# Kernel optimization log

Measured on AMD Instinct MI355X. Metric: run time of the kernel, lower is better.

## Reference

```python
import jax, jax.numpy as jnp
import numpy as np

N_COLS = 4096
N_ROWS = 4096
H = 64          # args.hidden1
S = 2           # per-edge supp feature count (cv_supp/vc_supp dim 0)
S_VO = 2        # vo_supp feature dim
S_CO = 2        # co_supp feature dim
EDGE_DENSITY = 0.03


def setup_inputs() -> dict:
    key = jax.random.key(0)
    ks = jax.random.split(key, 20)
    col_hidden = jax.random.normal(ks[0], (N_COLS, H), jnp.float32)
    row_hidden = jax.random.normal(ks[1], (N_ROWS, H), jnp.float32)
    obj_hidden = jax.random.normal(ks[2], (1, H), jnp.float32)
    # sparse bipartite adjacency encoded in supp[0] != 0 (as in the TF code)
    mask = jax.random.bernoulli(ks[3], EDGE_DENSITY, (N_ROWS, N_COLS))
    cv_supp = jax.random.normal(ks[4], (S, N_ROWS, N_COLS), jnp.float32) * mask[None]
    vc_supp = jnp.transpose(cv_supp, (0, 2, 1))  # [S, ncols, nrows]
    vo_supp = jax.random.normal(ks[5], (N_COLS, S_VO), jnp.float32)
    co_supp = jax.random.normal(ks[6], (N_ROWS, S_CO), jnp.float32)
    w = 0.05
    W_vo = jax.random.normal(ks[7], (2 * H, H), jnp.float32) * w
    W_oc = jax.random.normal(ks[8], (2 * H, H), jnp.float32) * w
    W_vc = jax.random.normal(ks[9], (2 * H, H), jnp.float32) * w
    W_co = jax.random.normal(ks[10], (2 * H, H), jnp.float32) * w
    W_ov = jax.random.normal(ks[11], (2 * H, H), jnp.float32) * w
    W_cv = jax.random.normal(ks[12], (2 * H, H), jnp.float32) * w
    # attention scorer nets: Dense(concat_dim -> 1) + sigmoid
    w_attn_vo = jax.random.normal(ks[13], (2 * H + S_VO, 1), jnp.float32) * 0.1
    b_attn_vo = jnp.zeros((), jnp.float32)
    w_attn_co = jax.random.normal(ks[14], (2 * H + S_CO, 1), jnp.float32) * 0.1
    b_attn_co = jnp.zeros((), jnp.float32)
    # pairwise attn nets decomposed into [col | supp | row] weight slices
    w_cv_col = jax.random.normal(ks[15], (H,), jnp.float32) * 0.1
    w_cv_supp = jax.random.normal(ks[16], (S,), jnp.float32) * 0.1
    w_cv_row = jax.random.normal(ks[17], (H,), jnp.float32) * 0.1
    b_cv = jnp.zeros((), jnp.float32)
    w_vc_row = jax.random.normal(ks[18], (H,), jnp.float32) * 0.1
    w_vc_supp = jax.random.normal(ks[19], (S,), jnp.float32) * 0.1
    w_vc_col = jax.random.normal(jax.random.fold_in(key, 99), (H,), jnp.float32) * 0.1
    b_vc = jnp.zeros((), jnp.float32)
    return dict(col_hidden=col_hidden, row_hidden=row_hidden, obj_hidden=obj_hidden,
                cv_supp=cv_supp, vc_supp=vc_supp, vo_supp=vo_supp, co_supp=co_supp,
                W_vo=W_vo, W_oc=W_oc, W_vc=W_vc, W_co=W_co, W_ov=W_ov, W_cv=W_cv,
                w_attn_vo=w_attn_vo, b_attn_vo=b_attn_vo,
                w_attn_co=w_attn_co, b_attn_co=b_attn_co,
                w_cv_col=w_cv_col, w_cv_supp=w_cv_supp, w_cv_row=w_cv_row, b_cv=b_cv,
                w_vc_row=w_vc_row, w_vc_supp=w_vc_supp, w_vc_col=w_vc_col, b_vc=b_vc)


def _forward(col_hidden, row_hidden, obj_hidden, cv_supp, vc_supp, vo_supp, co_supp,
             W_vo, W_oc, W_vc, W_co, W_ov, W_cv,
             w_attn_vo, b_attn_vo, w_attn_co, b_attn_co,
             w_cv_col, w_cv_supp, w_cv_row, b_cv,
             w_vc_row, w_vc_supp, w_vc_col, b_vc):
    act = jax.nn.relu
    ncols, nrows = col_hidden.shape[0], row_hidden.shape[0]
    # ---- v -> o: attend over all columns, update obj node ----
    vo_in = jnp.concatenate([col_hidden, vo_supp,
                             jnp.broadcast_to(obj_hidden, (ncols, H))], axis=1)
    a_vo = jax.nn.sigmoid(vo_in @ w_attn_vo + b_attn_vo)          # [ncols, 1]
    v_o_out = a_vo.T @ col_hidden                                  # [1, H]
    obj = act(jnp.concatenate([obj_hidden, v_o_out], axis=1) @ W_vo)
    # ---- v -> c: per-row ragged neighbor attention, vectorized via masked pairwise scores ----
    nbr_cv = cv_supp[0] != 0                                       # [nrows, ncols]
    logits_cv = ((row_hidden @ w_cv_row)[:, None]
                 + (col_hidden @ w_cv_col)[None, :]
                 + jnp.einsum('snc,s->nc', cv_supp, w_cv_supp) + b_cv)
    score_cv = jnp.where(nbr_cv, jax.nn.sigmoid(logits_cv), 0.0)   # [nrows, ncols]
    v_out = score_cv @ col_hidden                                  # [nrows, H]
    o_c_out = act(jnp.concatenate([jnp.broadcast_to(obj, (nrows, H)), row_hidden], axis=1) @ W_oc)
    row_next = act(jnp.concatenate([o_c_out, v_out], axis=1) @ W_vc)
    # ---- c -> o ----
    co_in = jnp.concatenate([row_next, co_supp,
                             jnp.broadcast_to(obj, (nrows, H))], axis=1)
    a_co = jax.nn.sigmoid(co_in @ w_attn_co + b_attn_co)           # [nrows, 1]
    c_o_out = a_co.T @ row_next                                    # [1, H]
    obj = act(jnp.concatenate([obj, c_o_out], axis=1) @ W_co)
    # ---- c -> v ----
    nbr_vc = vc_supp[0] != 0                                       # [ncols, nrows]
    logits_vc = ((col_hidden @ w_vc_col)[:, None]
                 + (row_next @ w_vc_row)[None, :]
                 + jnp.einsum('scn,s->cn', vc_supp, w_vc_supp) + b_vc)
    score_vc = jnp.where(nbr_vc, jax.nn.sigmoid(logits_vc), 0.0)   # [ncols, nrows]
    c_out = score_vc @ row_next                                    # [ncols, H]
    o_v_out = act(jnp.concatenate([jnp.broadcast_to(obj, (ncols, H)), col_hidden], axis=1) @ W_ov)
    col_next = act(jnp.concatenate([o_v_out, c_out], axis=1) @ W_cv)
    return col_next, row_next, obj


def reference(col_hidden, row_hidden, obj_hidden, cv_supp, vc_supp, vo_supp, co_supp,
              W_vo, W_oc, W_vc, W_co, W_ov, W_cv,
              w_attn_vo, b_attn_vo, w_attn_co, b_attn_co,
              w_cv_col, w_cv_supp, w_cv_row, b_cv,
              w_vc_row, w_vc_supp, w_vc_col, b_vc):
    col_next, row_next, obj = _forward(
        col_hidden, row_hidden, obj_hidden, cv_supp, vc_supp, vo_supp, co_supp,
        W_vo, W_oc, W_vc, W_co, W_ov, W_cv,
        w_attn_vo, b_attn_vo, w_attn_co, b_attn_co,
        w_cv_col, w_cv_supp, w_cv_row, b_cv,
        w_vc_row, w_vc_supp, w_vc_col, b_vc)
    # original layer also passes the supp tensors through unchanged
    return (col_next, row_next, obj, cv_supp, vc_supp, vo_supp, co_supp)
```

## Files before the change

kernel.cpp:

```cpp
#include <hip/hip_runtime.h>
#include <math.h>

typedef float f4 __attribute__((ext_vector_type(4)));

#define PLANE (4096*4096)

#define OUT_COL 0
#define OUT_ROW 262144
#define OUT_OBJ 524288
#define OUT_CV  524352
#define OUT_VC  34078784
#define OUT_VO  67633216
#define OUT_CO  67641408

#define WS_VO_P 0
#define WS_CO_P 1024
#define WS_OBJ1 2048
#define WS_RDCV 2112
#define WS_CDCV 6208
#define WS_RDVC 10304
#define WS_CDVC 14400
#define WS_PART 18496

__device__ __forceinline__ float sigf(float x) {
    return 1.0f / (1.0f + __expf(-x));
}

#define AS1 __attribute__((address_space(1)))
#define AS3 __attribute__((address_space(3)))
__device__ __forceinline__ void gl_lds16(const float* g, float* l) {
    __builtin_amdgcn_global_load_lds((const AS1 void*)g, (AS3 void*)l, 16, 0, 0);
}

#define SSWZ_F4C(row, f4c) ((f4c) ^ ((((row) >> 2) & 3) << 1))

__device__ __forceinline__ void attn_body(
    int blk, int t, const float* __restrict__ X, const float* __restrict__ supp,
    const float* __restrict__ obj, const float* __restrict__ wat,
    const float* __restrict__ bat, float* __restrict__ accP,
    const float* __restrict__ wextra, float* __restrict__ dextra,
    float* sA, float* sAcc)
{
    const int i = blk * 256 + t;
    float od = 0.f;
    for (int h = 0; h < 64; ++h) od += obj[h] * wat[66 + h];
    float x = bat[0] + od + supp[i*2] * wat[64] + supp[i*2+1] * wat[65];
    const f4* Xr = (const f4*)(X + i*64);
    f4 xd = 0.f, dd = 0.f;
    #pragma unroll
    for (int q = 0; q < 16; ++q) {
        f4 xv = Xr[q];
        xd += xv * ((const f4*)wat)[q];
        if (wextra) dd += xv * ((const f4*)wextra)[q];
    }
    x += xd.x + xd.y + xd.z + xd.w;
    if (dextra) dextra[i] = dd.x + dd.y + dd.z + dd.w;
    sA[t] = sigf(x);
    if (t < 64) sAcc[t] = 0.f;
    __syncthreads();
    const int w = t >> 6, h = t & 63;
    const int base = blk * 256 + w * 64;
    float partial = 0.f;
    for (int j = 0; j < 64; ++j)
        partial += sA[w*64 + j] * X[(base + j)*64 + h];
    atomicAdd(&sAcc[h], partial);
    __syncthreads();
    if (t < 64) accP[blk*64 + t] = sAcc[t];
}

__global__ __launch_bounds__(256) void k_front(
    const float* __restrict__ col_hidden, const float* __restrict__ row_hidden,
    const float* __restrict__ w_cv_col, const float* __restrict__ w_vc_col,
    const float* __restrict__ w_cv_row,
    float* __restrict__ cdcv, float* __restrict__ cdvc, float* __restrict__ rdcv,
    const float* __restrict__ vo_supp, const float* __restrict__ co_supp,
    float* __restrict__ out_vo, float* __restrict__ out_co,
    const float* __restrict__ obj_hidden, const float* __restrict__ w_attn_vo,
    const float* __restrict__ b_attn_vo, float* __restrict__ voP)
{
    __shared__ float sA[256];
    __shared__ float sAcc[64];
    const int t = threadIdx.x;
    if (blockIdx.x < 3072) {
        const int gw = blockIdx.x * 4 + (t >> 6);
        const int lane = t & 63;
        const int which = gw >> 12;
        const int row = gw & 4095;
        const float* x; const float* w; float* dst;
        if (which == 0)      { x = col_hidden; w = w_cv_col; dst = cdcv; }
        else if (which == 1) { x = col_hidden; w = w_vc_col; dst = cdvc; }
        else                 { x = row_hidden; w = w_cv_row; dst = rdcv; }
        float v = x[row * 64 + lane] * w[lane];
        #pragma unroll
        for (int off = 32; off; off >>= 1) v += __shfl_down(v, off, 64);
        if (lane == 0) dst[row] = v;
        return;
    }
    if (blockIdx.x < 3088) {
        const int idx = (blockIdx.x - 3072) * 256 + t;
        if (idx < 2048) ((f4*)out_vo)[idx] = ((const f4*)vo_supp)[idx];
        else            ((f4*)out_co)[idx - 2048] = ((const f4*)co_supp)[idx - 2048];
        return;
    }
    attn_body(blockIdx.x - 3088, t, col_hidden, vo_supp, obj_hidden,
              w_attn_vo, b_attn_vo, voP, nullptr, nullptr, sA, sAcc);
}

__global__ __launch_bounds__(256) void k_attn(
    const float* __restrict__ X, const float* __restrict__ supp,
    const float* __restrict__ obj, const float* __restrict__ wat,
    const float* __restrict__ bat, float* __restrict__ accP,
    const float* __restrict__ wextra, float* __restrict__ dextra)
{
    __shared__ float sA[256];
    __shared__ float sAcc[64];
    attn_body(blockIdx.x, threadIdx.x, X, supp, obj, wat, bat, accP,
              wextra, dextra, sA, sAcc);
}

__global__ __launch_bounds__(256, 2) void k_big(
    const float* __restrict__ supp0, const float* __restrict__ supp1,
    const float* __restrict__ Bm,
    const float* __restrict__ rdot, const float* __restrict__ cdot,
    const float* __restrict__ wsup, const float* __restrict__ bias,
    float* __restrict__ part, float* __restrict__ pass0, float* __restrict__ pass1,
    const float* __restrict__ objL, const float* __restrict__ objRp,
    const float* __restrict__ Wobj, float* __restrict__ objDst)
{
    __shared__ __align__(16) float lds0[64*128];
    __shared__ __align__(16) float lds1[64*128];
    const int t = threadIdx.x;

    if (blockIdx.x == 2048) {
        if (t < 64) {
            float r = 0.f;
            for (int b = 0; b < 16; ++b) r += objRp[b*64 + t];
            lds0[t] = r;
        }
        __syncthreads();
        if (t < 64) {
            float acc = 0.f;
            for (int k = 0; k < 64; ++k) acc += objL[k] * Wobj[k*64 + t];
            for (int k = 0; k < 64; ++k) acc += lds0[k] * Wobj[(64+k)*64 + t];
            objDst[t] = fmaxf(acc, 0.f);
        }
        return;
    }

    const int bi = blockIdx.x >> 5;
    const int bj = blockIdx.x & 31;
    const int i0 = bi * 64;
    const int jt0 = bj * 128;
    const int w = t >> 6, lane = t & 63;
    const float w0 = wsup[0], w1 = wsup[1], bv = bias[0];

    for (int k = 0; k < 8; ++k) {
        const int p = w * 8 + k;
        const size_t g = (size_t)(i0 + 2*p + (lane >> 5)) * 4096 + jt0 + (lane & 31) * 4;
        gl_lds16(supp0 + g, lds0 + p * 256);
        gl_lds16(supp1 + g, lds1 + p * 256);
    }
    __syncthreads();

    {
        const int f4c = lane & 31;
        const f4 cd = *(const f4*)(cdot + jt0 + f4c * 4);
        for (int q = 0; q < 8; ++q) {
            const int p = q * 4 + w;
            const int row = 2 * p + (lane >> 5);
            f4 a0 = *(const f4*)(lds0 + p * 256 + lane * 4);
            f4 a1 = *(const f4*)(lds1 + p * 256 + lane * 4);
            const size_t g = (size_t)(i0 + row) * 4096 + jt0 + f4c * 4;
            *(f4*)(pass0 + g) = a0;
            *(f4*)(pass1 + g) = a1;
            const float rd = rdot[i0 + row];
            f4 lg = rd + cd + w0 * a0 + w1 * a1 + bv;
            f4 s;
            s.x = (a0.x != 0.f) ? sigf(lg.x) : 0.f;
            s.y = (a0.y != 0.f) ? sigf(lg.y) : 0.f;
            s.z = (a0.z != 0.f) ? sigf(lg.z) : 0.f;
            s.w = (a0.w != 0.f) ? sigf(lg.w) : 0.f;
            *(f4*)(lds0 + row * 128 + SSWZ_F4C(row, f4c) * 4) = s;
        }
    }
    __syncthreads();

    for (int k = 0; k < 8; ++k) {
        const int c = w * 8 + k;
        gl_lds16(Bm + (size_t)(jt0 + c * 4) * 64 + lane * 4, lds1 + c * 256);
    }
    __syncthreads();

    const int ilb = t >> 4;
    const int hf4 = t & 15;
    const int sw  = (ilb & 3) << 1;
    f4 acc0 = 0.f, acc1 = 0.f, acc2 = 0.f, acc3 = 0.f;
    #pragma unroll 4
    for (int jf = 0; jf < 32; ++jf) {
        const int jj = jf * 4;
        f4 b0 = *(const f4*)(lds1 + (jj + 0) * 64 + hf4 * 4);
        f4 b1 = *(const f4*)(lds1 + (jj + 1) * 64 + hf4 * 4);
        f4 b2 = *(const f4*)(lds1 + (jj + 2) * 64 + hf4 * 4);
        f4 b3 = *(const f4*)(lds1 + (jj + 3) * 64 + hf4 * 4);
        const int sf = (jf ^ sw) * 4;
        { f4 s = *(const f4*)(lds0 + (ilb*4 + 0) * 128 + sf); acc0 += s.x*b0 + s.y*b1 + s.z*b2 + s.w*b3; }
        { f4 s = *(const f4*)(lds0 + (ilb*4 + 1) * 128 + sf); acc1 += s.x*b0 + s.y*b1 + s.z*b2 + s.w*b3; }
        { f4 s = *(const f4*)(lds0 + (ilb*4 + 2) * 128 + sf); acc2 += s.x*b0 + s.y*b1 + s.z*b2 + s.w*b3; }
        { f4 s = *(const f4*)(lds0 + (ilb*4 + 3) * 128 + sf); acc3 += s.x*b0 + s.y*b1 + s.z*b2 + s.w*b3; }
    }
    float* pb = part + (size_t)bj * 262144 + (size_t)i0 * 64;
    *(f4*)(pb + (ilb*4 + 0)*64 + hf4*4) = acc0;
    *(f4*)(pb + (ilb*4 + 1)*64 + hf4*4) = acc1;
    *(f4*)(pb + (ilb*4 + 2)*64 + hf4*4) = acc2;
    *(f4*)(pb + (ilb*4 + 3)*64 + hf4*4) = acc3;
}

__global__ __launch_bounds__(256) void k_mlp2(
    const float* __restrict__ objx, const float* __restrict__ base,
    const float* __restrict__ W1, const float* __restrict__ part,
    const float* __restrict__ W2, float* __restrict__ dst)
{
    __shared__ float mid[4][64];
    __shared__ float accs[4][64];
    const int t = threadIdx.x, w = t >> 6, h = t & 63;
    const int n = blockIdx.x * 4 + w;
    float v = 0.f;
    #pragma unroll 8
    for (int j = 0; j < 32; ++j) v += part[(size_t)j * 262144 + n*64 + h];
    accs[w][h] = v;
    float m = 0.f;
    for (int k = 0; k < 64; ++k) m += objx[k] * W1[k*64 + h];
    for (int k = 0; k < 64; ++k) m += base[n*64 + k] * W1[(64+k)*64 + h];
    mid[w][h] = fmaxf(m, 0.f);
    __syncthreads();
    float o = 0.f;
    for (int k = 0; k < 64; ++k) o += mid[w][k] * W2[k*64 + h];
    for (int k = 0; k < 64; ++k) o += accs[w][k] * W2[(64+k)*64 + h];
    dst[n*64 + h] = fmaxf(o, 0.f);
}

extern "C" void kernel_launch(void* const* d_in, const int* in_sizes, int n_in,
                              void* d_out, int out_size, void* d_ws, size_t ws_size,
                              hipStream_t stream)
{
    const float* col_hidden = (const float*)d_in[0];
    const float* row_hidden = (const float*)d_in[1];
    const float* obj_hidden = (const float*)d_in[2];
    const float* cv_supp    = (const float*)d_in[3];
    const float* vc_supp    = (const float*)d_in[4];
    const float* vo_supp    = (const float*)d_in[5];
    const float* co_supp    = (const float*)d_in[6];
    const float* W_vo       = (const float*)d_in[7];
    const float* W_oc       = (const float*)d_in[8];
    const float* W_vc       = (const float*)d_in[9];
    const float* W_co       = (const float*)d_in[10];
    const float* W_ov       = (const float*)d_in[11];
    const float* W_cv       = (const float*)d_in[12];
    const float* w_attn_vo  = (const float*)d_in[13];
    const float* b_attn_vo  = (const float*)d_in[14];
    const float* w_attn_co  = (const float*)d_in[15];
    const float* b_attn_co  = (const float*)d_in[16];
    const float* w_cv_col   = (const float*)d_in[17];
    const float* w_cv_supp  = (const float*)d_in[18];
    const float* w_cv_row   = (const float*)d_in[19];
    const float* b_cv       = (const float*)d_in[20];
    const float* w_vc_row   = (const float*)d_in[21];
    const float* w_vc_supp  = (const float*)d_in[22];
    const float* w_vc_col   = (const float*)d_in[23];
    const float* b_vc       = (const float*)d_in[24];

    float* out = (float*)d_out;
    float* ws  = (float*)d_ws;

    k_front<<<3104, 256, 0, stream>>>(col_hidden, row_hidden, w_cv_col, w_vc_col, w_cv_row,
                                      ws + WS_CDCV, ws + WS_CDVC, ws + WS_RDCV,
                                      vo_supp, co_supp, out + OUT_VO, out + OUT_CO,
                                      obj_hidden, w_attn_vo, b_attn_vo, ws + WS_VO_P);
    k_big<<<2049, 256, 0, stream>>>(cv_supp, cv_supp + PLANE, col_hidden,
                                    ws + WS_RDCV, ws + WS_CDCV, w_cv_supp, b_cv,
                                    ws + WS_PART, out + OUT_CV, out + OUT_CV + PLANE,
                                    obj_hidden, ws + WS_VO_P, W_vo, ws + WS_OBJ1);
    k_mlp2<<<1024, 256, 0, stream>>>(ws + WS_OBJ1, row_hidden, W_oc, ws + WS_PART, W_vc,
                                     out + OUT_ROW);
    k_attn<<<16, 256, 0, stream>>>(out + OUT_ROW, co_supp, ws + WS_OBJ1, w_attn_co, b_attn_co,
                                   ws + WS_CO_P, w_vc_row, ws + WS_RDVC);
    k_big<<<2049, 256, 0, stream>>>(vc_supp, vc_supp + PLANE, out + OUT_ROW,
                                    ws + WS_CDVC, ws + WS_RDVC, w_vc_supp, b_vc,
                                    ws + WS_PART, out + OUT_VC, out + OUT_VC + PLANE,
                                    ws + WS_OBJ1, ws + WS_CO_P, W_co, out + OUT_OBJ);
    k_mlp2<<<1024, 256, 0, stream>>>(out + OUT_OBJ, col_hidden, W_ov, ws + WS_PART, W_cv,
                                     out + OUT_COL);
}
```

Baseline: 577.2 us.

## Warp-specialize k_big into producer/consumer double-buffered persistent tiles

k_big now runs 256 blocks of 512 threads, each covering 8 column tiles in sequence. Producer waves load the supp tiles, compute the masked sigmoid scores and load the B tile into a double-buffered LDS slot, while consumer waves run the matmul on the previous slot. The goal is to overlap global loads and the sigmoid stage with the FMA work and cut block launch overhead. The attention helpers now use 64-row blocks to get more parallelism, and k_mlp2 reduces partials with vectorized loads split across warps. The trade-off is 128KB of LDS per block and only 256 blocks, which may leave some CUs idle or underfilled.

Result: no change. 585.8 us (+1.5%).

```diff
diff --git a/kernel.cpp b/kernel.cpp
--- a/kernel.cpp
+++ b/kernel.cpp
@@ -14,13 +14,13 @@
 #define OUT_CO  67641408
 
 #define WS_VO_P 0
-#define WS_CO_P 1024
-#define WS_OBJ1 2048
-#define WS_RDCV 2112
-#define WS_CDCV 6208
-#define WS_RDVC 10304
-#define WS_CDVC 14400
-#define WS_PART 18496
+#define WS_CO_P 4096
+#define WS_OBJ1 8192
+#define WS_RDCV 8256
+#define WS_CDCV 12352
+#define WS_RDVC 16448
+#define WS_CDVC 20544
+#define WS_PART 24640
 
 __device__ __forceinline__ float sigf(float x) {
     return 1.0f / (1.0f + __expf(-x));
@@ -32,38 +32,38 @@
     __builtin_amdgcn_global_load_lds((const AS1 void*)g, (AS3 void*)l, 16, 0, 0);
 }
 
-#define SSWZ_F4C(row, f4c) ((f4c) ^ ((((row) >> 2) & 3) << 1))
-
-__device__ __forceinline__ void attn_body(
+__device__ __forceinline__ void attn_body64(
     int blk, int t, const float* __restrict__ X, const float* __restrict__ supp,
     const float* __restrict__ obj, const float* __restrict__ wat,
     const float* __restrict__ bat, float* __restrict__ accP,
     const float* __restrict__ wextra, float* __restrict__ dextra,
     float* sA, float* sAcc)
 {
-    const int i = blk * 256 + t;
-    float od = 0.f;
-    for (int h = 0; h < 64; ++h) od += obj[h] * wat[66 + h];
-    float x = bat[0] + od + supp[i*2] * wat[64] + supp[i*2+1] * wat[65];
-    const f4* Xr = (const f4*)(X + i*64);
-    f4 xd = 0.f, dd = 0.f;
-    #pragma unroll
-    for (int q = 0; q < 16; ++q) {
-        f4 xv = Xr[q];
-        xd += xv * ((const f4*)wat)[q];
-        if (wextra) dd += xv * ((const f4*)wextra)[q];
-    }
-    x += xd.x + xd.y + xd.z + xd.w;
-    if (dextra) dextra[i] = dd.x + dd.y + dd.z + dd.w;
-    sA[t] = sigf(x);
-    if (t < 64) sAcc[t] = 0.f;
+    const int w = t >> 6, lane = t & 63;
+    if (t < 64) {
+        const int i = blk * 64 + t;
+        float od = 0.f;
+        for (int h = 0; h < 64; ++h) od += obj[h] * wat[66 + h];
+        float x = bat[0] + od + supp[i*2] * wat[64] + supp[i*2+1] * wat[65];
+        const f4* Xr = (const f4*)(X + i*64);
+        f4 xd = 0.f, dd = 0.f;
+        #pragma unroll
+        for (int q = 0; q < 16; ++q) {
+            f4 xv = Xr[q];
+            xd += xv * ((const f4*)wat)[q];
+            if (wextra) dd += xv * ((const f4*)wextra)[q];
+        }
+        x += xd.x + xd.y + xd.z + xd.w;
+        if (dextra) dextra[i] = dd.x + dd.y + dd.z + dd.w;
+        sA[t] = sigf(x);
+        sAcc[t] = 0.f;
+    }
     __syncthreads();
-    const int w = t >> 6, h = t & 63;
-    const int base = blk * 256 + w * 64;
     float partial = 0.f;
-    for (int j = 0; j < 64; ++j)
-        partial += sA[w*64 + j] * X[(base + j)*64 + h];
-    atomicAdd(&sAcc[h], partial);
+    const int jbase = blk * 64 + w * 16;
+    for (int j = 0; j < 16; ++j)
+        partial += sA[w*16 + j] * X[(jbase + j)*64 + lane];
+    atomicAdd(&sAcc[lane], partial);
     __syncthreads();
     if (t < 64) accP[blk*64 + t] = sAcc[t];
 }
@@ -78,7 +78,7 @@
     const float* __restrict__ obj_hidden, const float* __restrict__ w_attn_vo,
     const float* __restrict__ b_attn_vo, float* __restrict__ voP)
 {
-    __shared__ float sA[256];
+    __shared__ float sA[64];
     __shared__ float sAcc[64];
     const int t = threadIdx.x;
     if (blockIdx.x < 3072) {
@@ -102,8 +102,8 @@
         else            ((f4*)out_co)[idx - 2048] = ((const f4*)co_supp)[idx - 2048];
         return;
     }
-    attn_body(blockIdx.x - 3088, t, col_hidden, vo_supp, obj_hidden,
-              w_attn_vo, b_attn_vo, voP, nullptr, nullptr, sA, sAcc);
+    attn_body64(blockIdx.x - 3088, t, col_hidden, vo_supp, obj_hidden,
+                w_attn_vo, b_attn_vo, voP, nullptr, nullptr, sA, sAcc);
 }
 
 __global__ __launch_bounds__(256) void k_attn(
@@ -112,13 +112,13 @@
     const float* __restrict__ bat, float* __restrict__ accP,
     const float* __restrict__ wextra, float* __restrict__ dextra)
 {
-    __shared__ float sA[256];
+    __shared__ float sA[64];
     __shared__ float sAcc[64];
-    attn_body(blockIdx.x, threadIdx.x, X, supp, obj, wat, bat, accP,
-              wextra, dextra, sA, sAcc);
-}
-
-__global__ __launch_bounds__(256, 2) void k_big(
+    attn_body64(blockIdx.x, threadIdx.x, X, supp, obj, wat, bat, accP,
+                wextra, dextra, sA, sAcc);
+}
+
+__global__ __launch_bounds__(512, 2) void k_big(
     const float* __restrict__ supp0, const float* __restrict__ supp1,
     const float* __restrict__ Bm,
     const float* __restrict__ rdot, const float* __restrict__ cdot,
@@ -127,92 +127,101 @@
     const float* __restrict__ objL, const float* __restrict__ objRp,
     const float* __restrict__ Wobj, float* __restrict__ objDst)
 {
-    __shared__ __align__(16) float lds0[64*128];
-    __shared__ __align__(16) float lds1[64*128];
+    __shared__ __align__(16) float lds[2][2][8192];
     const int t = threadIdx.x;
 
-    if (blockIdx.x == 2048) {
+    if (blockIdx.x == 256) {
         if (t < 64) {
             float r = 0.f;
-            for (int b = 0; b < 16; ++b) r += objRp[b*64 + t];
-            lds0[t] = r;
+            for (int b = 0; b < 64; ++b) r += objRp[b*64 + t];
+            lds[0][0][t] = r;
         }
         __syncthreads();
         if (t < 64) {
             float acc = 0.f;
             for (int k = 0; k < 64; ++k) acc += objL[k] * Wobj[k*64 + t];
-            for (int k = 0; k < 64; ++k) acc += lds0[k] * Wobj[(64+k)*64 + t];
+            for (int k = 0; k < 64; ++k) acc += lds[0][0][k] * Wobj[(64+k)*64 + t];
             objDst[t] = fmaxf(acc, 0.f);
         }
         return;
     }
 
-    const int bi = blockIdx.x >> 5;
-    const int bj = blockIdx.x & 31;
+    const int bi = blockIdx.x >> 2;
+    const int jg = blockIdx.x & 3;
     const int i0 = bi * 64;
-    const int jt0 = bj * 128;
     const int w = t >> 6, lane = t & 63;
     const float w0 = wsup[0], w1 = wsup[1], bv = bias[0];
-
-    for (int k = 0; k < 8; ++k) {
-        const int p = w * 8 + k;
-        const size_t g = (size_t)(i0 + 2*p + (lane >> 5)) * 4096 + jt0 + (lane & 31) * 4;
-        gl_lds16(supp0 + g, lds0 + p * 256);
-        gl_lds16(supp1 + g, lds1 + p * 256);
-    }
-    __syncthreads();
-
-    {
-        const int f4c = lane & 31;
-        const f4 cd = *(const f4*)(cdot + jt0 + f4c * 4);
-        for (int q = 0; q < 8; ++q) {
-            const int p = q * 4 + w;
-            const int row = 2 * p + (lane >> 5);
-            f4 a0 = *(const f4*)(lds0 + p * 256 + lane * 4);
-            f4 a1 = *(const f4*)(lds1 + p * 256 + lane * 4);
-            const size_t g = (size_t)(i0 + row) * 4096 + jt0 + f4c * 4;
-            *(f4*)(pass0 + g) = a0;
-            *(f4*)(pass1 + g) = a1;
-            const float rd = rdot[i0 + row];
-            f4 lg = rd + cd + w0 * a0 + w1 * a1 + bv;
-            f4 s;
-            s.x = (a0.x != 0.f) ? sigf(lg.x) : 0.f;
-            s.y = (a0.y != 0.f) ? sigf(lg.y) : 0.f;
-            s.z = (a0.z != 0.f) ? sigf(lg.z) : 0.f;
-            s.w = (a0.w != 0.f) ? sigf(lg.w) : 0.f;
-            *(f4*)(lds0 + row * 128 + SSWZ_F4C(row, f4c) * 4) = s;
+    const bool producer = (w >= 4);
+    const int pw = w & 3;
+
+    for (int it = 0; it <= 8; ++it) {
+        if (producer && it < 8) {
+            float* s0 = &lds[it & 1][0][0];
+            float* s1 = &lds[it & 1][1][0];
+            const int jt0 = (jg * 8 + it) * 128;
+            for (int k = 0; k < 8; ++k) {
+                const int p = pw + 4 * k;
+                const size_t g = (size_t)(i0 + 2*p + (lane >> 5)) * 4096 + jt0 + (lane & 31) * 4;
+                gl_lds16(supp0 + g, s0 + p * 256);
+                gl_lds16(supp1 + g, s1 + p * 256);
+            }
+            asm volatile("s_waitcnt vmcnt(0)" ::: "memory");
+            __builtin_amdgcn_sched_barrier(0);
+            const int c4 = (lane & 31) * 4;
+            const f4 cd = *(const f4*)(cdot + jt0 + c4);
+            for (int q = 0; q < 8; ++q) {
+                const int p = q * 4 + pw;
+                const int row = 2 * p + (lane >> 5);
+                f4 a0 = *(const f4*)(s0 + row * 128 + c4);
+                f4 a1 = *(const f4*)(s1 + row * 128 + c4);
+                const size_t g = (size_t)(i0 + row) * 4096 + jt0 + c4;
+                *(f4*)(pass0 + g) = a0;
+                *(f4*)(pass1 + g) = a1;
+                const float rd = rdot[i0 + row];
+                f4 lg = rd + cd + w0*a0 + w1*a1 + bv;
+                f4 s;
+                s.x = (a0.x != 0.f) ? sigf(lg.x) : 0.f;
+                s.y = (a0.y != 0.f) ? sigf(lg.y) : 0.f;
+                s.z = (a0.z != 0.f) ? sigf(lg.z) : 0.f;
+                s.w = (a0.w != 0.f) ? sigf(lg.w) : 0.f;
+                const int swz = (lane & 31) ^ (((row >> 2) & 3) << 1);
+                *(f4*)(s0 + row * 128 + swz * 4) = s;
+            }
+            asm volatile("s_waitcnt lgkmcnt(0)" ::: "memory");
+            __builtin_amdgcn_sched_barrier(0);
+            for (int k = 0; k < 8; ++k) {
+                const int c = pw + 4 * k;
+                gl_lds16(Bm + (size_t)(jt0 + c * 4) * 64 + lane * 4, s1 + c * 256);
+            }
+        } else if (!producer && it >= 1) {
+            const float* s0 = &lds[(it - 1) & 1][0][0];
+            const float* s1 = &lds[(it - 1) & 1][1][0];
+            const int ilb = t >> 4;
+            const int hf4 = t & 15;
+            const int sw  = (ilb & 3) << 1;
+            f4 acc0 = 0.f, acc1 = 0.f, acc2 = 0.f, acc3 = 0.f;
+            #pragma unroll 4
+            for (int jf = 0; jf < 32; ++jf) {
+                const int jj = jf * 4;
+                f4 b0 = *(const f4*)(s1 + (jj + 0) * 64 + hf4 * 4);
+                f4 b1 = *(const f4*)(s1 + (jj + 1) * 64 + hf4 * 4);
+                f4 b2 = *(const f4*)(s1 + (jj + 2) * 64 + hf4 * 4);
+                f4 b3 = *(const f4*)(s1 + (jj + 3) * 64 + hf4 * 4);
+                const int sf = (jf ^ sw) * 4;
+                { f4 s = *(const f4*)(s0 + (ilb*4 + 0) * 128 + sf); acc0 += s.x*b0 + s.y*b1 + s.z*b2 + s.w*b3; }
+                { f4 s = *(const f4*)(s0 + (ilb*4 + 1) * 128 + sf); acc1 += s.x*b0 + s.y*b1 + s.z*b2 + s.w*b3; }
+                { f4 s = *(const f4*)(s0 + (ilb*4 + 2) * 128 + sf); acc2 += s.x*b0 + s.y*b1 + s.z*b2 + s.w*b3; }
+                { f4 s = *(const f4*)(s0 + (ilb*4 + 3) * 128 + sf); acc3 += s.x*b0 + s.y*b1 + s.z*b2 + s.w*b3; }
+            }
+            const int js = jg * 8 + (it - 1);
+            float* pb = part + (size_t)js * 262144 + (size_t)i0 * 64;
+            *(f4*)(pb + (ilb*4 + 0)*64 + hf4*4) = acc0;
+            *(f4*)(pb + (ilb*4 + 1)*64 + hf4*4) = acc1;
+            *(f4*)(pb + (ilb*4 + 2)*64 + hf4*4) = acc2;
+            *(f4*)(pb + (ilb*4 + 3)*64 + hf4*4) = acc3;
         }
-    }
-    __syncthreads();
-
-    for (int k = 0; k < 8; ++k) {
-        const int c = w * 8 + k;
-        gl_lds16(Bm + (size_t)(jt0 + c * 4) * 64 + lane * 4, lds1 + c * 256);
-    }
-    __syncthreads();
-
-    const int ilb = t >> 4;
-    const int hf4 = t & 15;
-    const int sw  = (ilb & 3) << 1;
-    f4 acc0 = 0.f, acc1 = 0.f, acc2 = 0.f, acc3 = 0.f;
-    #pragma unroll 4
-    for (int jf = 0; jf < 32; ++jf) {
-        const int jj = jf * 4;
-        f4 b0 = *(const f4*)(lds1 + (jj + 0) * 64 + hf4 * 4);
-        f4 b1 = *(const f4*)(lds1 + (jj + 1) * 64 + hf4 * 4);
-        f4 b2 = *(const f4*)(lds1 + (jj + 2) * 64 + hf4 * 4);
-        f4 b3 = *(const f4*)(lds1 + (jj + 3) * 64 + hf4 * 4);
-        const int sf = (jf ^ sw) * 4;
-        { f4 s = *(const f4*)(lds0 + (ilb*4 + 0) * 128 + sf); acc0 += s.x*b0 + s.y*b1 + s.z*b2 + s.w*b3; }
-        { f4 s = *(const f4*)(lds0 + (ilb*4 + 1) * 128 + sf); acc1 += s.x*b0 + s.y*b1 + s.z*b2 + s.w*b3; }
-        { f4 s = *(const f4*)(lds0 + (ilb*4 + 2) * 128 + sf); acc2 += s.x*b0 + s.y*b1 + s.z*b2 + s.w*b3; }
-        { f4 s = *(const f4*)(lds0 + (ilb*4 + 3) * 128 + sf); acc3 += s.x*b0 + s.y*b1 + s.z*b2 + s.w*b3; }
-    }
-    float* pb = part + (size_t)bj * 262144 + (size_t)i0 * 64;
-    *(f4*)(pb + (ilb*4 + 0)*64 + hf4*4) = acc0;
-    *(f4*)(pb + (ilb*4 + 1)*64 + hf4*4) = acc1;
-    *(f4*)(pb + (ilb*4 + 2)*64 + hf4*4) = acc2;
-    *(f4*)(pb + (ilb*4 + 3)*64 + hf4*4) = acc3;
+        __syncthreads();
+    }
 }
 
 __global__ __launch_bounds__(256) void k_mlp2(
@@ -221,22 +230,25 @@
     const float* __restrict__ W2, float* __restrict__ dst)
 {
     __shared__ float mid[4][64];
+    __shared__ float accsP[4][256];
     __shared__ float accs[4][64];
-    const int t = threadIdx.x, w = t >> 6, h = t & 63;
-    const int n = blockIdx.x * 4 + w;
-    float v = 0.f;
-    #pragma unroll 8
-    for (int j = 0; j < 32; ++j) v += part[(size_t)j * 262144 + n*64 + h];
-    accs[w][h] = v;
+    const int t = threadIdx.x, w = t >> 6, h = t & 63, lane = t & 63;
+    const int nbase = blockIdx.x * 4;
+    f4 v = 0.f;
+    for (int j = w; j < 32; j += 4)
+        v += *(const f4*)(part + (size_t)j * 262144 + blockIdx.x * 256 + lane * 4);
+    *(f4*)&accsP[w][lane * 4] = v;
     float m = 0.f;
     for (int k = 0; k < 64; ++k) m += objx[k] * W1[k*64 + h];
-    for (int k = 0; k < 64; ++k) m += base[n*64 + k] * W1[(64+k)*64 + h];
+    for (int k = 0; k < 64; ++k) m += base[(nbase + w)*64 + k] * W1[(64+k)*64 + h];
     mid[w][h] = fmaxf(m, 0.f);
+    __syncthreads();
+    accs[t >> 6][t & 63] = accsP[0][t] + accsP[1][t] + accsP[2][t] + accsP[3][t];
     __syncthreads();
     float o = 0.f;
     for (int k = 0; k < 64; ++k) o += mid[w][k] * W2[k*64 + h];
     for (int k = 0; k < 64; ++k) o += accs[w][k] * W2[(64+k)*64 + h];
-    dst[n*64 + h] = fmaxf(o, 0.f);
+    dst[(nbase + w)*64 + h] = fmaxf(o, 0.f);
 }
 
 extern "C" void kernel_launch(void* const* d_in, const int* in_sizes, int n_in,
@@ -272,22 +284,22 @@
     float* out = (float*)d_out;
     float* ws  = (float*)d_ws;
 
-    k_front<<<3104, 256, 0, stream>>>(col_hidden, row_hidden, w_cv_col, w_vc_col, w_cv_row,
+    k_front<<<3152, 256, 0, stream>>>(col_hidden, row_hidden, w_cv_col, w_vc_col, w_cv_row,
                                       ws + WS_CDCV, ws + WS_CDVC, ws + WS_RDCV,
                                       vo_supp, co_supp, out + OUT_VO, out + OUT_CO,
                                       obj_hidden, w_attn_vo, b_attn_vo, ws + WS_VO_P);
-    k_big<<<2049, 256, 0, stream>>>(cv_supp, cv_supp + PLANE, col_hidden,
-                                    ws + WS_RDCV, ws + WS_CDCV, w_cv_supp, b_cv,
-                                    ws + WS_PART, out + OUT_CV, out + OUT_CV + PLANE,
-                                    obj_hidden, ws + WS_VO_P, W_vo, ws + WS_OBJ1);
+    k_big<<<257, 512, 0, stream>>>(cv_supp, cv_supp + PLANE, col_hidden,
+                                   ws + WS_RDCV, ws + WS_CDCV, w_cv_supp, b_cv,
+                                   ws + WS_PART, out + OUT_CV, out + OUT_CV + PLANE,
+                                   obj_hidden, ws + WS_VO_P, W_vo, ws + WS_OBJ1);
     k_mlp2<<<1024, 256, 0, stream>>>(ws + WS_OBJ1, row_hidden, W_oc, ws + WS_PART, W_vc,
                                      out + OUT_ROW);
-    k_attn<<<16, 256, 0, stream>>>(out + OUT_ROW, co_supp, ws + WS_OBJ1, w_attn_co, b_attn_co,
+    k_attn<<<64, 256, 0, stream>>>(out + OUT_ROW, co_supp, ws + WS_OBJ1, w_attn_co, b_attn_co,
                                    ws + WS_CO_P, w_vc_row, ws + WS_RDVC);
-    k_big<<<2049, 256, 0, stream>>>(vc_supp, vc_supp + PLANE, out + OUT_ROW,
-                                    ws + WS_CDVC, ws + WS_RDVC, w_vc_supp, b_vc,
-                                    ws + WS_PART, out + OUT_VC, out + OUT_VC + PLANE,
-                                    ws + WS_OBJ1, ws + WS_CO_P, W_co, out + OUT_OBJ);
+    k_big<<<257, 512, 0, stream>>>(vc_supp, vc_supp + PLANE, out + OUT_ROW,
+                                   ws + WS_CDVC, ws + WS_RDVC, w_vc_supp, b_vc,
+                                   ws + WS_PART, out + OUT_VC, out + OUT_VC + PLANE,
+                                   ws + WS_OBJ1, ws + WS_CO_P, W_co, out + OUT_OBJ);
     k_mlp2<<<1024, 256, 0, stream>>>(out + OUT_OBJ, col_hidden, W_ov, ws + WS_PART, W_cv,
                                      out + OUT_COL);
 }
```
